# Optimization experiments

Measured on AMD Instinct MI355X. Metric: run time of the kernel, lower is better.

## Reference

```python
import jax, jax.numpy as jnp
import numpy as np

B, D, H, W = 2, 256, 64, 64
NH = 4
EPS = 1e-5


def _ln(x, g, b):
    # LayerNorm over channel dim of NCHW tensor (matches permute->LN(C)->permute)
    mu = jnp.mean(x, axis=1, keepdims=True)
    var = jnp.mean((x - mu) ** 2, axis=1, keepdims=True)
    xn = (x - mu) * jax.lax.rsqrt(var + EPS)
    return xn * g[None, :, None, None] + b[None, :, None, None]


def _conv1x1(x, w, b):
    # w: (out_c, in_c)
    return jnp.einsum('bchw,oc->bohw', x, w) + b[None, :, None, None]


def _dwconv3x3(x, w, b):
    # depthwise 3x3, w: (C, 1, 3, 3)
    y = jax.lax.conv_general_dilated(
        x, w, window_strides=(1, 1), padding='SAME',
        dimension_numbers=('NCHW', 'OIHW', 'NCHW'), feature_group_count=D)
    return y + b[None, :, None, None]


def setup_inputs() -> dict:
    key = jax.random.key(0)
    ks = jax.random.split(key, 12)
    sc = 0.02

    def n(k, shape):
        return jax.random.normal(k, shape, dtype=jnp.float32) * sc

    return {
        'image_embedding': jax.random.normal(ks[0], (B, D, H, W), dtype=jnp.float32),
        'guide': jax.random.normal(ks[1], (B, D, H, W), dtype=jnp.float32),
        'ln1_g': jnp.ones((D,), jnp.float32), 'ln1_b': jnp.zeros((D,), jnp.float32),
        'ln2_g': jnp.ones((D,), jnp.float32), 'ln2_b': jnp.zeros((D,), jnp.float32),
        'qw1': n(ks[2], (D, D)), 'qb1': jnp.zeros((D,), jnp.float32),
        'qw2': n(ks[3], (D, 1, 3, 3)), 'qb2': jnp.zeros((D,), jnp.float32),
        'kw1': n(ks[4], (D, D)), 'kb1': jnp.zeros((D,), jnp.float32),
        'kw2': n(ks[5], (D, 1, 3, 3)), 'kb2': jnp.zeros((D,), jnp.float32),
        'vw1': n(ks[6], (D, D)), 'vb1': jnp.zeros((D,), jnp.float32),
        'vw2': n(ks[7], (D, 1, 3, 3)), 'vb2': jnp.zeros((D,), jnp.float32),
        'ow': n(ks[8], (D, D)), 'ob': jnp.zeros((D,), jnp.float32),
    }


def reference(image_embedding, guide, ln1_g, ln1_b, ln2_g, ln2_b,
              qw1, qb1, qw2, qb2, kw1, kb1, kw2, kb2,
              vw1, vb1, vw2, vb2, ow, ob):
    residual = image_embedding
    x = _ln(image_embedding, ln1_g, ln1_b)
    g = _ln(guide, ln2_g, ln2_b)

    q = _dwconv3x3(_conv1x1(x, qw1, qb1), qw2, qb2)
    k = _dwconv3x3(_conv1x1(g, kw1, kb1), kw2, kb2)
    v = _dwconv3x3(_conv1x1(g, vw1, vb1), vw2, vb2)

    hd = D // NH
    scale = hd ** -0.5

    def to_heads(t):  # (B,C,H,W) -> (B, NH, HW, hd)
        return t.reshape(B, NH, hd, H * W).transpose(0, 1, 3, 2)

    q = to_heads(q) * scale
    k = to_heads(k)
    v = to_heads(v)

    attn = jax.nn.softmax(jnp.einsum('bhnd,bhmd->bhnm', q, k), axis=-1)
    out = jnp.einsum('bhnm,bhmd->bhnd', attn, v)
    out = out.transpose(0, 1, 3, 2).reshape(B, D, H, W)
    out = _conv1x1(out, ow, ob)
    return residual + out
```

## Files before the change

### kernel.cpp

```cpp
#include <hip/hip_runtime.h>
#include <cstdint>
#include <cstddef>

typedef unsigned short u16;
typedef unsigned int u32;
typedef __attribute__((ext_vector_type(8))) short short8;
typedef __attribute__((ext_vector_type(4))) float f32x4;
typedef __attribute__((ext_vector_type(16))) float f32x16;
typedef __attribute__((ext_vector_type(2))) unsigned int u32x2;

#define CD 256
#define HWD 4096
#define NHD 4
#define HDD 64
#define NSPLIT 4

static __device__ __forceinline__ u16 f2b(float f) {
    u32 u = __builtin_bit_cast(u32, f);
    return (u16)((u + 0x7fffu + ((u >> 16) & 1u)) >> 16);
}
static __device__ __forceinline__ float b2f(u16 h) {
    return __builtin_bit_cast(float, (u32)h << 16);
}
static __device__ __forceinline__ u32 pk2(float a, float b) {
    return (u32)f2b(a) | ((u32)f2b(b) << 16);
}
static __device__ __forceinline__ float fexp2(float x) {
#if __has_builtin(__builtin_amdgcn_exp2f)
    return __builtin_amdgcn_exp2f(x);
#else
    return __expf(x * 0.69314718056f);
#endif
}
static __device__ __forceinline__ u32 cvtpk(float lo, float hi) {
    u32 r;
    asm("v_cvt_pk_bf16_f32 %0, %1, %2" : "=v"(r) : "v"(lo), "v"(hi));
    return r;
}
static __device__ __forceinline__ u32x2 plswap(u32 a, u32 b) {
    return __builtin_amdgcn_permlane32_swap(a, b, false, false);
}
static __device__ __forceinline__ void async16(const void* g, void* l) {
    __builtin_amdgcn_global_load_lds(
        (const __attribute__((address_space(1))) unsigned int*)g,
        (__attribute__((address_space(3))) unsigned int*)l,
        16, 0, 0);
}

__global__ __launch_bounds__(256) void ln_transpose(
    const float* __restrict__ x0, const float* __restrict__ x1,
    const float* __restrict__ g0, const float* __restrict__ b0,
    const float* __restrict__ g1, const float* __restrict__ b1,
    const float* __restrict__ qw1, const float* __restrict__ kw1,
    const float* __restrict__ vw1, const float* __restrict__ ow,
    u16* __restrict__ out0, u16* __restrict__ out1, u16* __restrict__ wbf)
{
    int bid = blockIdx.x;
    int tid = threadIdx.x;

    if (bid >= 512) {
        int base = (bid - 512) * 8192 + tid * 32;
        int which = base >> 16;
        int off = base & 65535;
        const float* s = (which == 0) ? qw1 : (which == 1) ? kw1
                       : (which == 2) ? vw1 : ow;
        s += off;
        u16* d = wbf + (size_t)which * 65536 + off;
        #pragma unroll
        for (int j = 0; j < 4; ++j) {
            float4 a = ((const float4*)s)[2 * j];
            float4 b = ((const float4*)s)[2 * j + 1];
            uint4 o;
            o.x = pk2(a.x, a.y); o.y = pk2(a.z, a.w);
            o.z = pk2(b.x, b.y); o.w = pk2(b.z, b.w);
            ((uint4*)d)[j] = o;
        }
        return;
    }

    int t = bid >> 8, b = (bid >> 7) & 1, p0 = (bid & 127) << 5;
    const float* x = t ? x1 : x0;
    const float* g = t ? g1 : g0;
    const float* bb = t ? b1 : b0;
    u16* out = t ? out1 : out0;

    int tx = tid & 31, ty = tid >> 5;
    const float* xb = x + (size_t)b * CD * HWD + p0 + tx;

    __shared__ float red[2][8][32];
    __shared__ u16 T[256][33];

    float xv[32];
    float s = 0.f, sq = 0.f;
    #pragma unroll
    for (int i = 0; i < 32; ++i) {
        float v = xb[(size_t)(ty * 32 + i) * HWD];
        xv[i] = v;
        s += v; sq += v * v;
    }
    red[0][ty][tx] = s; red[1][ty][tx] = sq;
    __syncthreads();
    float st = 0.f, sqt = 0.f;
    #pragma unroll
    for (int j = 0; j < 8; ++j) { st += red[0][j][tx]; sqt += red[1][j][tx]; }
    float mean = st * (1.f / 256.f);
    float var = sqt * (1.f / 256.f) - mean * mean;
    float rstd = rsqrtf(var + 1e-5f);

    #pragma unroll
    for (int i = 0; i < 32; ++i) {
        int c = ty * 32 + i;
        float v = (xv[i] - mean) * rstd * g[c] + bb[c];
        T[c][tx] = f2b(v);
    }
    __syncthreads();

    #pragma unroll
    for (int pass = 0; pass < 4; ++pass) {
        int idx = pass * 256 + tid;
        int p = idx >> 5, cs = (idx & 31) * 8;
        u16 tmp[8];
        #pragma unroll
        for (int j = 0; j < 8; ++j) tmp[j] = T[cs + j][p];
        *(uint4*)&out[((size_t)b * HWD + p0 + p) * CD + cs] = *(const uint4*)tmp;
    }
}

__global__ __launch_bounds__(256) void qkv_gemm(
    const u16* __restrict__ xT, const u16* __restrict__ gT,
    const u16* __restrict__ Wbf,
    const float* __restrict__ qb1, const float* __restrict__ kb1,
    const float* __restrict__ vb1,
    u16* __restrict__ q1, u16* __restrict__ k1, u16* __restrict__ v1)
{
    int z = blockIdx.z;
    int mm = z >> 1, b = z & 1;
    const u16* X    = (mm == 0) ? xT : gT;
    const u16* W    = Wbf + (size_t)mm * 65536;
    const float* Bi = (mm == 0) ? qb1 : (mm == 1) ? kb1 : vb1;
    u16* Y          = (mm == 0) ? q1 : (mm == 1) ? k1 : v1;

    int n0 = blockIdx.x * 128;
    int p0 = blockIdx.y * 32;

    __shared__ u16 As[32][72];
    __shared__ u16 Bs[128][72];

    int tid = threadIdx.x;
    int lane = tid & 63, w = tid >> 6;
    int l15 = lane & 15, quad = lane >> 4;

    f32x4 acc[2][2];
    #pragma unroll
    for (int mi = 0; mi < 2; ++mi)
        #pragma unroll
        for (int nj = 0; nj < 2; ++nj)
            acc[mi][nj] = (f32x4){0.f, 0.f, 0.f, 0.f};

    const u16* Xb = X + (size_t)b * HWD * CD;

    int arow = tid >> 3, aseg = (tid & 7) * 8;
    const u16* agp = Xb + (size_t)(p0 + arow) * CD + aseg;
    int brow = tid >> 1, bkh = (tid & 1) * 32;
    const u16* wgp = W + (size_t)(n0 + brow) * CD + bkh;

    uint4 ra0 = ((const uint4*)agp)[0];
    uint4 rb0 = ((const uint4*)wgp)[0], rb1 = ((const uint4*)wgp)[1];
    uint4 rb2 = ((const uint4*)wgp)[2], rb3 = ((const uint4*)wgp)[3];

    for (int kt = 0; kt < 4; ++kt) {
        __syncthreads();
        *(uint4*)&As[arow][aseg] = ra0;
        *(uint4*)&Bs[brow][bkh] = rb0;
        *(uint4*)&Bs[brow][bkh + 8] = rb1;
        *(uint4*)&Bs[brow][bkh + 16] = rb2;
        *(uint4*)&Bs[brow][bkh + 24] = rb3;
        if (kt < 3) {
            ra0 = *(const uint4*)(agp + (kt + 1) * 64);
            const u16* wg2 = wgp + (kt + 1) * 64;
            rb0 = ((const uint4*)wg2)[0]; rb1 = ((const uint4*)wg2)[1];
            rb2 = ((const uint4*)wg2)[2]; rb3 = ((const uint4*)wg2)[3];
        }
        __syncthreads();

        #pragma unroll
        for (int kk = 0; kk < 2; ++kk) {
            short8 af[2], bf[2];
            #pragma unroll
            for (int mi = 0; mi < 2; ++mi)
                af[mi] = *(const short8*)&As[mi * 16 + l15][kk * 32 + quad * 8];
            #pragma unroll
            for (int nj = 0; nj < 2; ++nj)
                bf[nj] = *(const short8*)&Bs[w * 32 + nj * 16 + l15][kk * 32 + quad * 8];
            #pragma unroll
            for (int mi = 0; mi < 2; ++mi)
                #pragma unroll
                for (int nj = 0; nj < 2; ++nj)
                    acc[mi][nj] = __builtin_amdgcn_mfma_f32_16x16x32_bf16(
                        af[mi], bf[nj], acc[mi][nj], 0, 0, 0);
        }
    }

    u16* Yb = Y + (size_t)b * HWD * CD;
    float bias[2];
    #pragma unroll
    for (int nj = 0; nj < 2; ++nj)
        bias[nj] = Bi[n0 + w * 32 + nj * 16 + l15];
    #pragma unroll
    for (int mi = 0; mi < 2; ++mi) {
        #pragma unroll
        for (int r = 0; r < 4; ++r) {
            int p = p0 + mi * 16 + quad * 4 + r;
            #pragma unroll
            for (int nj = 0; nj < 2; ++nj) {
                int ch = n0 + w * 32 + nj * 16 + l15;
                Yb[(size_t)p * CD + ch] = f2b(acc[mi][nj][r] + bias[nj]);
            }
        }
    }
}

#define LOADROW(r, hh)                                                      \
    if ((hh) < 0 || (hh) >= 64) {                                           \
        _Pragma("unroll") for (int j = 0; j < 18; ++j) r[j] = 0.f;          \
    } else {                                                                \
        const u16* rp = inb + (size_t)((hh) * 64) * CD;                     \
        r[0] = (w0 > 0) ? b2f(rp[(size_t)(w0 - 1) * CD]) : 0.f;             \
        _Pragma("unroll") for (int j = 1; j <= 16; ++j)                     \
            r[j] = b2f(rp[(size_t)(w0 - 1 + j) * CD]);                      \
        r[17] = (w0 < 48) ? b2f(rp[(size_t)(w0 + 16) * CD]) : 0.f;          \
    }

#define CONVROW(hh, ra, rb, rc)                                             \
    {                                                                       \
        float accv[16];                                                     \
        _Pragma("unroll") for (int pi = 0; pi < 16; ++pi)                   \
            accv[pi] = bias                                                 \
              + w9[0] * ra[pi] + w9[1] * ra[pi + 1] + w9[2] * ra[pi + 2]    \
              + w9[3] * rb[pi] + w9[4] * rb[pi + 1] + w9[5] * rb[pi + 2]    \
              + w9[6] * rc[pi] + w9[7] * rc[pi + 1] + w9[8] * rc[pi + 2];   \
        int p0 = (hh) * 64 + w0;                                            \
        if (which == 2) {                                                   \
            u32 w8[8];                                                      \
            _Pragma("unroll") for (int j = 0; j < 8; ++j)                   \
                w8[j] = pk2(accv[2 * j], accv[2 * j + 1]);                  \
            uint4* dst = (uint4*)(Vt + ((size_t)(b * CD + c)) * HWD + p0);  \
            dst[0] = make_uint4(w8[0], w8[1], w8[2], w8[3]);                \
            dst[1] = make_uint4(w8[4], w8[5], w8[6], w8[7]);                \
        } else {                                                            \
            u16* outp = ((which == 0) ? Q : K) + (size_t)b * HWD * CD;      \
            _Pragma("unroll") for (int pi = 0; pi < 16; ++pi)               \
                outp[(size_t)(p0 + pi) * CD + c] = f2b(accv[pi] * oscale);  \
        }                                                                   \
    }

__global__ __launch_bounds__(256) void dwconv_nc(
    const u16* __restrict__ q1, const u16* __restrict__ k1, const u16* __restrict__ v1,
    const float* __restrict__ qw2, const float* __restrict__ qb2,
    const float* __restrict__ kw2, const float* __restrict__ kb2,
    const float* __restrict__ vw2, const float* __restrict__ vb2,
    u16* __restrict__ Q, u16* __restrict__ K, u16* __restrict__ Vt)
{
    int bid = blockIdx.x;
    int which = bid >> 8;
    int rem = bid & 255;
    int b = rem >> 7;
    int hp = (rem >> 2) & 31;
    int ws = rem & 3;
    int h0 = hp * 2, w0 = ws * 16;

    const u16* in = ((which == 0) ? q1 : (which == 1) ? k1 : v1) + (size_t)b * HWD * CD;
    const float* wsrc = (which == 0) ? qw2 : (which == 1) ? kw2 : vw2;
    const float* bsrc = (which == 0) ? qb2 : (which == 1) ? kb2 : vb2;
    float oscale = (which == 0) ? 0.18033688011112042f : 1.0f;

    int c = threadIdx.x;
    float w9[9];
    #pragma unroll
    for (int j = 0; j < 9; ++j) w9[j] = wsrc[c * 9 + j];
    float bias = bsrc[c];

    const u16* inb = in + c;

    float r0[18], r1[18], r2[18];
    LOADROW(r0, h0 - 1)
    LOADROW(r1, h0)
    LOADROW(r2, h0 + 1)
    CONVROW(h0, r0, r1, r2)
    LOADROW(r0, h0 + 2)
    CONVROW(h0 + 1, r1, r2, r0)
}

__global__ __launch_bounds__(256, 2) void attn_kernel(
    const u16* __restrict__ Q, const u16* __restrict__ K,
    const u16* __restrict__ Vt, u16* __restrict__ Opart,
    float* __restrict__ Psum)
{
    int qt = blockIdx.x;
    int bh = blockIdx.y;
    int ks = blockIdx.z;
    int b = bh >> 2, nh = bh & 3;

    __shared__ u16 Ks_[2][64 * 64];
    __shared__ u16 Vs_[2][64 * 64];

    int tid = threadIdx.x;
    int lane = tid & 63, w = tid >> 6;
    int l31 = lane & 31, h = lane >> 5;
    int sw = l31 & 7;

    const u16* Qb = Q + ((size_t)b * HWD) * CD + nh * 64;
    const u16* Kb = K + ((size_t)b * HWD) * CD + nh * 64;
    const u16* Vb = Vt + ((size_t)bh * HDD) * HWD;

    int q0 = qt * 256 + w * 64;

    short8 qf[2][4];
    #pragma unroll
    for (int qi = 0; qi < 2; ++qi)
        #pragma unroll
        for (int si = 0; si < 4; ++si)
            qf[qi][si] = *(const short8*)(Qb +
                (size_t)(q0 + qi * 32 + l31) * CD + si * 16 + h * 8);

    int rr = lane >> 3;
    int gseg = (lane & 7) ^ rr;
    const u16* kgb = Kb + (size_t)(ks * 1024 + w * 16 + rr) * CD + gseg * 8;
    const u16* vgb = Vb + (size_t)(w * 16 + rr) * HWD + ks * 1024 + gseg * 8;

    f32x16 acc[2][2];
    #pragma unroll
    for (int qi = 0; qi < 2; ++qi)
        #pragma unroll
        for (int db = 0; db < 2; ++db)
            #pragma unroll
            for (int r = 0; r < 16; ++r) acc[qi][db][r] = 0.f;
    float psum[2] = {0.f, 0.f};

    #pragma unroll
    for (int j = 0; j < 2; ++j) {
        async16(kgb + (size_t)(j * 8) * CD, &Ks_[0][(w * 16 + j * 8) * 64]);
        async16(vgb + (size_t)(j * 8) * HWD, &Vs_[0][(w * 16 + j * 8) * 64]);
    }

    for (int it = 0; it < 16; ++it) {
        int cur = it & 1;
        __syncthreads();
        if (it + 1 < 16) {
            int nxt = cur ^ 1;
            #pragma unroll
            for (int j = 0; j < 2; ++j) {
                async16(kgb + (size_t)((it + 1) * 64 + j * 8) * CD,
                        &Ks_[nxt][(w * 16 + j * 8) * 64]);
                async16(vgb + (size_t)(j * 8) * HWD + (it + 1) * 64,
                        &Vs_[nxt][(w * 16 + j * 8) * 64]);
            }
        }

        #pragma unroll
        for (int kb = 0; kb < 2; ++kb) {
            short8 kf[4];
            #pragma unroll
            for (int si = 0; si < 4; ++si)
                kf[si] = *(const short8*)&Ks_[cur][(kb * 32 + l31) * 64 +
                                                   (((si * 2 + h) ^ sw) << 3)];
            short8 vf[4];
            #pragma unroll
            for (int dz = 0; dz < 4; ++dz)
                vf[dz] = *(const short8*)&Vs_[cur][((dz >> 1) * 32 + l31) * 64 +
                             ((((kb * 2 + (dz & 1)) * 2 + h) ^ sw) << 3)];

            #pragma unroll
            for (int qi = 0; qi < 2; ++qi) {
                f32x16 st;
                #pragma unroll
                for (int r = 0; r < 16; ++r) st[r] = 0.f;
                __builtin_amdgcn_s_setprio(1);
                #pragma unroll
                for (int si = 0; si < 4; ++si)
                    st = __builtin_amdgcn_mfma_f32_32x32x16_bf16(
                        kf[si], qf[qi][si], st, 0, 0, 0);
                __builtin_amdgcn_s_setprio(0);

                float e[16];
                #pragma unroll
                for (int r = 0; r < 16; ++r) e[r] = fexp2(st[r]);
                #pragma unroll
                for (int r = 0; r < 16; r += 4)
                    psum[qi] += (e[r] + e[r + 1]) + (e[r + 2] + e[r + 3]);

                u32 wv[8];
                #pragma unroll
                for (int m = 0; m < 8; ++m) wv[m] = cvtpk(e[2 * m], e[2 * m + 1]);
                u32x2 s02 = plswap(wv[0], wv[2]);
                u32x2 s13 = plswap(wv[1], wv[3]);
                u32x2 s46 = plswap(wv[4], wv[6]);
                u32x2 s57 = plswap(wv[5], wv[7]);
                union { u32 u[4]; short8 s8; } p0_, p1_;
                p0_.u[0] = s02.x; p0_.u[1] = s13.x; p0_.u[2] = s02.y; p0_.u[3] = s13.y;
                p1_.u[0] = s46.x; p1_.u[1] = s57.x; p1_.u[2] = s46.y; p1_.u[3] = s57.y;

                __builtin_amdgcn_s_setprio(1);
                acc[qi][0] = __builtin_amdgcn_mfma_f32_32x32x16_bf16(
                    p0_.s8, vf[0], acc[qi][0], 0, 0, 0);
                acc[qi][0] = __builtin_amdgcn_mfma_f32_32x32x16_bf16(
                    p1_.s8, vf[1], acc[qi][0], 0, 0, 0);
                acc[qi][1] = __builtin_amdgcn_mfma_f32_32x32x16_bf16(
                    p0_.s8, vf[2], acc[qi][1], 0, 0, 0);
                acc[qi][1] = __builtin_amdgcn_mfma_f32_32x32x16_bf16(
                    p1_.s8, vf[3], acc[qi][1], 0, 0, 0);
                __builtin_amdgcn_s_setprio(0);
            }
        }
    }

    u16* Ob = Opart + (((size_t)ks * 8 + bh) * HWD) * HDD;
    #pragma unroll
    for (int qi = 0; qi < 2; ++qi)
        #pragma unroll
        for (int db = 0; db < 2; ++db)
            #pragma unroll
            for (int r = 0; r < 16; ++r) {
                int n = q0 + qi * 32 + (r & 3) + 8 * (r >> 2) + 4 * h;
                Ob[(size_t)n * HDD + db * 32 + l31] = f2b(acc[qi][db][r]);
            }

    float* Pb = Psum + ((size_t)ks * 8 + bh) * HWD + q0;
    #pragma unroll
    for (int qi = 0; qi < 2; ++qi) {
        float s = psum[qi] + __shfl_xor(psum[qi], 32);
        if (lane < 32) Pb[qi * 32 + lane] = s;
    }
}

__global__ __launch_bounds__(256) void out_gemm(
    const u16* __restrict__ Wo, const float* __restrict__ Bi,
    const u16* __restrict__ Opart, const float* __restrict__ Psum,
    const float* __restrict__ residual, float* __restrict__ out)
{
    int b = blockIdx.z;
    int m0 = blockIdx.y * 64;
    int n0 = blockIdx.x * 32;

    __shared__ u16 As[64][40];
    __shared__ u16 Bs[32][40];

    int tid = threadIdx.x;
    int lane = tid & 63, w = tid >> 6;
    int wm = w >> 1, wn = w & 1;
    int l15 = lane & 15, quad = lane >> 4;

    f32x4 acc[2];
    #pragma unroll
    for (int mi = 0; mi < 2; ++mi)
        acc[mi] = (f32x4){0.f, 0.f, 0.f, 0.f};

    int arow = tid >> 2, aseg = (tid & 3) * 8;
    const u16* wgp = Wo + (size_t)(m0 + arow) * CD + aseg;
    int brow = tid >> 3, bseg = (tid & 7) * 4;
    int pn = n0 + brow;

    uint4 ra = *(const uint4*)wgp;

    uint2 ro[NSPLIT]; float rinv;
    {
        int c = bseg;
        int bh = b * 4 + (c >> 6), d0 = c & 63;
        float p = 0.f;
        #pragma unroll
        for (int s = 0; s < NSPLIT; ++s) {
            ro[s] = *(const uint2*)&Opart[(((size_t)s * 8 + bh) * HWD + pn) * HDD + d0];
            p += Psum[((size_t)s * 8 + bh) * HWD + pn];
        }
        rinv = 1.f / p;
    }

    for (int kt = 0; kt < 8; ++kt) {
        __syncthreads();
        *(uint4*)&As[arow][aseg] = ra;
        {
            float v[4];
            #pragma unroll
            for (int j = 0; j < 4; ++j) v[j] = 0.f;
            #pragma unroll
            for (int s = 0; s < NSPLIT; ++s) {
                u16 t[4];
                *(uint2*)t = ro[s];
                #pragma unroll
                for (int j = 0; j < 4; ++j) v[j] += b2f(t[j]);
            }
            uint2 bb;
            bb.x = pk2(v[0] * rinv, v[1] * rinv);
            bb.y = pk2(v[2] * rinv, v[3] * rinv);
            *(uint2*)&Bs[brow][bseg] = bb;
        }
        if (kt < 7) {
            ra = *(const uint4*)(wgp + (kt + 1) * 32);
            int c = (kt + 1) * 32 + bseg;
            int bh = b * 4 + (c >> 6), d0 = c & 63;
            float p = 0.f;
            #pragma unroll
            for (int s = 0; s < NSPLIT; ++s) {
                ro[s] = *(const uint2*)&Opart[(((size_t)s * 8 + bh) * HWD + pn) * HDD + d0];
                p += Psum[((size_t)s * 8 + bh) * HWD + pn];
            }
            rinv = 1.f / p;
        }
        __syncthreads();

        short8 af[2], bf;
        #pragma unroll
        for (int mi = 0; mi < 2; ++mi)
            af[mi] = *(const short8*)&As[wm * 32 + mi * 16 + l15][quad * 8];
        bf = *(const short8*)&Bs[wn * 16 + l15][quad * 8];
        #pragma unroll
        for (int mi = 0; mi < 2; ++mi)
            acc[mi] = __builtin_amdgcn_mfma_f32_16x16x32_bf16(
                af[mi], bf, acc[mi], 0, 0, 0);
    }

    #pragma unroll
    for (int mi = 0; mi < 2; ++mi) {
        int mb = m0 + wm * 32 + mi * 16 + quad * 4;
        #pragma unroll
        for (int r = 0; r < 4; ++r) {
            float bias = Bi[mb + r];
            const float* res = residual + (size_t)(b * CD + mb + r) * HWD;
            float* o = out + (size_t)(b * CD + mb + r) * HWD;
            int n = n0 + wn * 16 + l15;
            o[n] = acc[mi][r] + bias + res[n];
        }
    }
}

extern "C" void kernel_launch(void* const* d_in, const int* in_sizes, int n_in,
                              void* d_out, int out_size, void* d_ws, size_t ws_size,
                              hipStream_t stream) {
    (void)in_sizes; (void)n_in; (void)out_size; (void)ws_size;

    const float* image = (const float*)d_in[0];
    const float* guide = (const float*)d_in[1];
    const float* ln1_g = (const float*)d_in[2];
    const float* ln1_b = (const float*)d_in[3];
    const float* ln2_g = (const float*)d_in[4];
    const float* ln2_b = (const float*)d_in[5];
    const float* qw1 = (const float*)d_in[6];
    const float* qb1 = (const float*)d_in[7];
    const float* qw2 = (const float*)d_in[8];
    const float* qb2 = (const float*)d_in[9];
    const float* kw1 = (const float*)d_in[10];
    const float* kb1 = (const float*)d_in[11];
    const float* kw2 = (const float*)d_in[12];
    const float* kb2 = (const float*)d_in[13];
    const float* vw1 = (const float*)d_in[14];
    const float* vb1 = (const float*)d_in[15];
    const float* vw2 = (const float*)d_in[16];
    const float* vb2 = (const float*)d_in[17];
    const float* ow  = (const float*)d_in[18];
    const float* ob  = (const float*)d_in[19];
    float* out = (float*)d_out;

    char* ws = (char*)d_ws;
    u16* xT    = (u16*)(ws + (size_t)0  * (1 << 20));
    u16* gT    = (u16*)(ws + (size_t)4  * (1 << 20));
    u16* q1    = (u16*)(ws + (size_t)8  * (1 << 20));
    u16* k1    = (u16*)(ws + (size_t)12 * (1 << 20));
    u16* v1    = (u16*)(ws + (size_t)16 * (1 << 20));
    u16* Qh    = (u16*)(ws + (size_t)20 * (1 << 20));
    u16* Kh    = (u16*)(ws + (size_t)24 * (1 << 20));
    u16* Vt    = (u16*)(ws + (size_t)28 * (1 << 20));
    u16*   Opart = (u16*)(ws + (size_t)0  * (1 << 20));
    float* Psum  = (float*)(ws + (size_t)18 * (1 << 20));
    u16*   Wbf   = (u16*)(ws + (size_t)33 * (1 << 20));

    ln_transpose<<<dim3(544), dim3(256), 0, stream>>>(
        image, guide, ln1_g, ln1_b, ln2_g, ln2_b,
        qw1, kw1, vw1, ow, xT, gT, Wbf);

    qkv_gemm<<<dim3(2, 128, 6), dim3(256), 0, stream>>>(
        xT, gT, Wbf, qb1, kb1, vb1, q1, k1, v1);

    dwconv_nc<<<dim3(768), dim3(256), 0, stream>>>(
        q1, k1, v1, qw2, qb2, kw2, kb2, vw2, vb2, Qh, Kh, Vt);

    attn_kernel<<<dim3(16, 8, NSPLIT), dim3(256), 0, stream>>>(Qh, Kh, Vt, Opart, Psum);

    out_gemm<<<dim3(128, 4, 2), dim3(256), 0, stream>>>(
        Wbf + (size_t)3 * 65536, ob, Opart, Psum, image, out);
}
```

Baseline: 174.6 us.

## Double-buffer QKV GEMM tiles with async global-to-LDS loads and XOR swizzle

The QKV projection GEMM now copies its A and B tiles straight from global memory into LDS with async 16-byte loads into two ping-pong buffers. This removes the register staging step and one barrier per k-step, so the next tile's loads overlap with the MFMA work on the current one. The padded LDS rows are replaced by an XOR-swizzled unpadded layout to avoid bank conflicts on the fragment reads. The swizzle is applied on the global-address side, and correctness depends on the barrier also waiting for the async loads to finish.

```diff
diff --git a/kernel.cpp b/kernel.cpp
--- a/kernel.cpp
+++ b/kernel.cpp
@@ -143,12 +143,22 @@
     int n0 = blockIdx.x * 128;
     int p0 = blockIdx.y * 32;
 
-    __shared__ u16 As[32][72];
-    __shared__ u16 Bs[128][72];
+    __shared__ u16 As[2][32 * 64];
+    __shared__ u16 Bs[2][128 * 64];
 
     int tid = threadIdx.x;
     int lane = tid & 63, w = tid >> 6;
     int l15 = lane & 15, quad = lane >> 4;
+    int sw = l15 & 7;
+
+    int srow = tid >> 3;
+    int sseg = tid & 7;
+    const u16* Xb = X + (size_t)b * HWD * CD;
+    const u16* agp = Xb + (size_t)(p0 + srow) * CD + (sseg ^ (srow & 7)) * 8;
+    const u16* wgp0 = W + (size_t)(n0 +  0 + srow) * CD + (sseg ^ (srow & 7)) * 8;
+    const u16* wgp1 = W + (size_t)(n0 + 32 + srow) * CD + (sseg ^ (srow & 7)) * 8;
+    const u16* wgp2 = W + (size_t)(n0 + 64 + srow) * CD + (sseg ^ (srow & 7)) * 8;
+    const u16* wgp3 = W + (size_t)(n0 + 96 + srow) * CD + (sseg ^ (srow & 7)) * 8;
 
     f32x4 acc[2][2];
     #pragma unroll
@@ -157,41 +167,39 @@
         for (int nj = 0; nj < 2; ++nj)
             acc[mi][nj] = (f32x4){0.f, 0.f, 0.f, 0.f};
 
-    const u16* Xb = X + (size_t)b * HWD * CD;
-
-    int arow = tid >> 3, aseg = (tid & 7) * 8;
-    const u16* agp = Xb + (size_t)(p0 + arow) * CD + aseg;
-    int brow = tid >> 1, bkh = (tid & 1) * 32;
-    const u16* wgp = W + (size_t)(n0 + brow) * CD + bkh;
-
-    uint4 ra0 = ((const uint4*)agp)[0];
-    uint4 rb0 = ((const uint4*)wgp)[0], rb1 = ((const uint4*)wgp)[1];
-    uint4 rb2 = ((const uint4*)wgp)[2], rb3 = ((const uint4*)wgp)[3];
+    async16(agp, &As[0][w * 512]);
+    async16(wgp0, &Bs[0][0 * 2048 + w * 512]);
+    async16(wgp1, &Bs[0][1 * 2048 + w * 512]);
+    async16(wgp2, &Bs[0][2 * 2048 + w * 512]);
+    async16(wgp3, &Bs[0][3 * 2048 + w * 512]);
 
     for (int kt = 0; kt < 4; ++kt) {
+        int cur = kt & 1;
         __syncthreads();
-        *(uint4*)&As[arow][aseg] = ra0;
-        *(uint4*)&Bs[brow][bkh] = rb0;
-        *(uint4*)&Bs[brow][bkh + 8] = rb1;
-        *(uint4*)&Bs[brow][bkh + 16] = rb2;
-        *(uint4*)&Bs[brow][bkh + 24] = rb3;
         if (kt < 3) {
-            ra0 = *(const uint4*)(agp + (kt + 1) * 64);
-            const u16* wg2 = wgp + (kt + 1) * 64;
-            rb0 = ((const uint4*)wg2)[0]; rb1 = ((const uint4*)wg2)[1];
-            rb2 = ((const uint4*)wg2)[2]; rb3 = ((const uint4*)wg2)[3];
-        }
-        __syncthreads();
+            int nxt = cur ^ 1;
+            async16(agp + (kt + 1) * 64, &As[nxt][w * 512]);
+            async16(wgp0 + (kt + 1) * 64, &Bs[nxt][0 * 2048 + w * 512]);
+            async16(wgp1 + (kt + 1) * 64, &Bs[nxt][1 * 2048 + w * 512]);
+            async16(wgp2 + (kt + 1) * 64, &Bs[nxt][2 * 2048 + w * 512]);
+            async16(wgp3 + (kt + 1) * 64, &Bs[nxt][3 * 2048 + w * 512]);
+        }
 
         #pragma unroll
         for (int kk = 0; kk < 2; ++kk) {
             short8 af[2], bf[2];
             #pragma unroll
-            for (int mi = 0; mi < 2; ++mi)
-                af[mi] = *(const short8*)&As[mi * 16 + l15][kk * 32 + quad * 8];
-            #pragma unroll
-            for (int nj = 0; nj < 2; ++nj)
-                bf[nj] = *(const short8*)&Bs[w * 32 + nj * 16 + l15][kk * 32 + quad * 8];
+            for (int mi = 0; mi < 2; ++mi) {
+                int row = mi * 16 + l15;
+                af[mi] = *(const short8*)&As[cur][row * 64 +
+                                                  (((kk * 4 + quad) ^ sw) << 3)];
+            }
+            #pragma unroll
+            for (int nj = 0; nj < 2; ++nj) {
+                int row = w * 32 + nj * 16 + l15;
+                bf[nj] = *(const short8*)&Bs[cur][row * 64 +
+                                                  (((kk * 4 + quad) ^ sw) << 3)];
+            }
             #pragma unroll
             for (int mi = 0; mi < 2; ++mi)
                 #pragma unroll
```

New measurement: 173.6 us, median of 2. About the same (-0.6%).

## Fuse LayerNorm into QKV GEMM and move output weight conversion to dwconv

Applied to the files above, without the earlier changes.

LayerNorm is now computed inside the QKV GEMM. Each block normalizes its 32-pixel tile over all 256 channels into a swizzled LDS buffer, and fp32 weights are converted to bf16 on the fly, so the separate transpose kernel and its xT/gT round trip go away. Conversion of the output-projection weight moves to extra blocks in the dwconv launch. This saves one kernel launch and the intermediate global traffic. In exchange, the LN is recomputed redundantly across the two n-blocks, across the k and v GEMMs, and across batches per z, and weight conversion is repeated per block.

```diff
diff --git a/kernel.cpp b/kernel.cpp
--- a/kernel.cpp
+++ b/kernel.cpp
@@ -47,108 +47,75 @@
         16, 0, 0);
 }
 
-__global__ __launch_bounds__(256) void ln_transpose(
+__global__ __launch_bounds__(256) void ln_qkv_gemm(
     const float* __restrict__ x0, const float* __restrict__ x1,
     const float* __restrict__ g0, const float* __restrict__ b0,
     const float* __restrict__ g1, const float* __restrict__ b1,
     const float* __restrict__ qw1, const float* __restrict__ kw1,
-    const float* __restrict__ vw1, const float* __restrict__ ow,
-    u16* __restrict__ out0, u16* __restrict__ out1, u16* __restrict__ wbf)
-{
-    int bid = blockIdx.x;
-    int tid = threadIdx.x;
-
-    if (bid >= 512) {
-        int base = (bid - 512) * 8192 + tid * 32;
-        int which = base >> 16;
-        int off = base & 65535;
-        const float* s = (which == 0) ? qw1 : (which == 1) ? kw1
-                       : (which == 2) ? vw1 : ow;
-        s += off;
-        u16* d = wbf + (size_t)which * 65536 + off;
-        #pragma unroll
-        for (int j = 0; j < 4; ++j) {
-            float4 a = ((const float4*)s)[2 * j];
-            float4 b = ((const float4*)s)[2 * j + 1];
-            uint4 o;
-            o.x = pk2(a.x, a.y); o.y = pk2(a.z, a.w);
-            o.z = pk2(b.x, b.y); o.w = pk2(b.z, b.w);
-            ((uint4*)d)[j] = o;
-        }
-        return;
-    }
-
-    int t = bid >> 8, b = (bid >> 7) & 1, p0 = (bid & 127) << 5;
-    const float* x = t ? x1 : x0;
-    const float* g = t ? g1 : g0;
-    const float* bb = t ? b1 : b0;
-    u16* out = t ? out1 : out0;
-
-    int tx = tid & 31, ty = tid >> 5;
-    const float* xb = x + (size_t)b * CD * HWD + p0 + tx;
-
-    __shared__ float red[2][8][32];
-    __shared__ u16 T[256][33];
-
-    float xv[32];
-    float s = 0.f, sq = 0.f;
-    #pragma unroll
-    for (int i = 0; i < 32; ++i) {
-        float v = xb[(size_t)(ty * 32 + i) * HWD];
-        xv[i] = v;
-        s += v; sq += v * v;
-    }
-    red[0][ty][tx] = s; red[1][ty][tx] = sq;
-    __syncthreads();
-    float st = 0.f, sqt = 0.f;
-    #pragma unroll
-    for (int j = 0; j < 8; ++j) { st += red[0][j][tx]; sqt += red[1][j][tx]; }
-    float mean = st * (1.f / 256.f);
-    float var = sqt * (1.f / 256.f) - mean * mean;
-    float rstd = rsqrtf(var + 1e-5f);
-
-    #pragma unroll
-    for (int i = 0; i < 32; ++i) {
-        int c = ty * 32 + i;
-        float v = (xv[i] - mean) * rstd * g[c] + bb[c];
-        T[c][tx] = f2b(v);
-    }
-    __syncthreads();
-
-    #pragma unroll
-    for (int pass = 0; pass < 4; ++pass) {
-        int idx = pass * 256 + tid;
-        int p = idx >> 5, cs = (idx & 31) * 8;
-        u16 tmp[8];
-        #pragma unroll
-        for (int j = 0; j < 8; ++j) tmp[j] = T[cs + j][p];
-        *(uint4*)&out[((size_t)b * HWD + p0 + p) * CD + cs] = *(const uint4*)tmp;
-    }
-}
-
-__global__ __launch_bounds__(256) void qkv_gemm(
-    const u16* __restrict__ xT, const u16* __restrict__ gT,
-    const u16* __restrict__ Wbf,
+    const float* __restrict__ vw1,
     const float* __restrict__ qb1, const float* __restrict__ kb1,
     const float* __restrict__ vb1,
     u16* __restrict__ q1, u16* __restrict__ k1, u16* __restrict__ v1)
 {
     int z = blockIdx.z;
     int mm = z >> 1, b = z & 1;
-    const u16* X    = (mm == 0) ? xT : gT;
-    const u16* W    = Wbf + (size_t)mm * 65536;
+    const float* x  = (mm == 0) ? x0 : x1;
+    const float* g  = (mm == 0) ? g0 : g1;
+    const float* bb = (mm == 0) ? b0 : b1;
+    const float* W  = (mm == 0) ? qw1 : (mm == 1) ? kw1 : vw1;
     const float* Bi = (mm == 0) ? qb1 : (mm == 1) ? kb1 : vb1;
     u16* Y          = (mm == 0) ? q1 : (mm == 1) ? k1 : v1;
 
     int n0 = blockIdx.x * 128;
     int p0 = blockIdx.y * 32;
 
-    __shared__ u16 As[32][72];
+    __shared__ u16 As[32 * 256];
     __shared__ u16 Bs[128][72];
+    __shared__ float red[2][8][32];
 
     int tid = threadIdx.x;
     int lane = tid & 63, w = tid >> 6;
     int l15 = lane & 15, quad = lane >> 4;
+    int sw = l15 & 7;
+
+    int tx = tid & 31, ty = tid >> 5;
+    const float* xb = x + (size_t)b * CD * HWD + p0 + tx;
+    float xv[32];
+    float s = 0.f, sq = 0.f;
+    #pragma unroll
+    for (int i = 0; i < 32; ++i) {
+        float v = xb[(size_t)(ty * 32 + i) * HWD];
+        xv[i] = v; s += v; sq += v * v;
+    }
+    red[0][ty][tx] = s; red[1][ty][tx] = sq;
+    __syncthreads();
+    float st = 0.f, sqt = 0.f;
+    #pragma unroll
+    for (int j = 0; j < 8; ++j) { st += red[0][j][tx]; sqt += red[1][j][tx]; }
+    float mean = st * (1.f / 256.f);
+    float var = sqt * (1.f / 256.f) - mean * mean;
+    float rstd = rsqrtf(var + 1e-5f);
+
+    #pragma unroll
+    for (int j = 0; j < 4; ++j) {
+        float v[8];
+        #pragma unroll
+        for (int e = 0; e < 8; ++e) {
+            int c = ty * 32 + j * 8 + e;
+            v[e] = (xv[j * 8 + e] - mean) * rstd * g[c] + bb[c];
+        }
+        uint4 o;
+        o.x = pk2(v[0], v[1]); o.y = pk2(v[2], v[3]);
+        o.z = pk2(v[4], v[5]); o.w = pk2(v[6], v[7]);
+        int chunk = (ty * 4 + j) ^ (tx & 7);
+        *(uint4*)&As[tx * 256 + chunk * 8] = o;
+    }
+
+    int brow = tid >> 1, bkh = (tid & 1) * 32;
+    const float* wgp = W + (size_t)(n0 + brow) * CD + bkh;
+    float4 rw[8];
+    #pragma unroll
+    for (int j = 0; j < 8; ++j) rw[j] = ((const float4*)wgp)[j];
 
     f32x4 acc[2][2];
     #pragma unroll
@@ -157,29 +124,27 @@
         for (int nj = 0; nj < 2; ++nj)
             acc[mi][nj] = (f32x4){0.f, 0.f, 0.f, 0.f};
 
-    const u16* Xb = X + (size_t)b * HWD * CD;
-
-    int arow = tid >> 3, aseg = (tid & 7) * 8;
-    const u16* agp = Xb + (size_t)(p0 + arow) * CD + aseg;
-    int brow = tid >> 1, bkh = (tid & 1) * 32;
-    const u16* wgp = W + (size_t)(n0 + brow) * CD + bkh;
-
-    uint4 ra0 = ((const uint4*)agp)[0];
-    uint4 rb0 = ((const uint4*)wgp)[0], rb1 = ((const uint4*)wgp)[1];
-    uint4 rb2 = ((const uint4*)wgp)[2], rb3 = ((const uint4*)wgp)[3];
-
     for (int kt = 0; kt < 4; ++kt) {
         __syncthreads();
-        *(uint4*)&As[arow][aseg] = ra0;
-        *(uint4*)&Bs[brow][bkh] = rb0;
-        *(uint4*)&Bs[brow][bkh + 8] = rb1;
-        *(uint4*)&Bs[brow][bkh + 16] = rb2;
-        *(uint4*)&Bs[brow][bkh + 24] = rb3;
+        {
+            uint4 qa, qb;
+            qa.x = pk2(rw[0].x, rw[0].y); qa.y = pk2(rw[0].z, rw[0].w);
+            qa.z = pk2(rw[1].x, rw[1].y); qa.w = pk2(rw[1].z, rw[1].w);
+            qb.x = pk2(rw[2].x, rw[2].y); qb.y = pk2(rw[2].z, rw[2].w);
+            qb.z = pk2(rw[3].x, rw[3].y); qb.w = pk2(rw[3].z, rw[3].w);
+            *(uint4*)&Bs[brow][bkh] = qa;
+            *(uint4*)&Bs[brow][bkh + 8] = qb;
+            qa.x = pk2(rw[4].x, rw[4].y); qa.y = pk2(rw[4].z, rw[4].w);
+            qa.z = pk2(rw[5].x, rw[5].y); qa.w = pk2(rw[5].z, rw[5].w);
+            qb.x = pk2(rw[6].x, rw[6].y); qb.y = pk2(rw[6].z, rw[6].w);
+            qb.z = pk2(rw[7].x, rw[7].y); qb.w = pk2(rw[7].z, rw[7].w);
+            *(uint4*)&Bs[brow][bkh + 16] = qa;
+            *(uint4*)&Bs[brow][bkh + 24] = qb;
+        }
         if (kt < 3) {
-            ra0 = *(const uint4*)(agp + (kt + 1) * 64);
-            const u16* wg2 = wgp + (kt + 1) * 64;
-            rb0 = ((const uint4*)wg2)[0]; rb1 = ((const uint4*)wg2)[1];
-            rb2 = ((const uint4*)wg2)[2]; rb3 = ((const uint4*)wg2)[3];
+            const float* wg2 = wgp + (kt + 1) * 64;
+            #pragma unroll
+            for (int j = 0; j < 8; ++j) rw[j] = ((const float4*)wg2)[j];
         }
         __syncthreads();
 
@@ -187,8 +152,11 @@
         for (int kk = 0; kk < 2; ++kk) {
             short8 af[2], bf[2];
             #pragma unroll
-            for (int mi = 0; mi < 2; ++mi)
-                af[mi] = *(const short8*)&As[mi * 16 + l15][kk * 32 + quad * 8];
+            for (int mi = 0; mi < 2; ++mi) {
+                int row = mi * 16 + l15;
+                int c = kt * 8 + kk * 4 + quad;
+                af[mi] = *(const short8*)&As[row * 256 + ((c ^ sw) << 3)];
+            }
             #pragma unroll
             for (int nj = 0; nj < 2; ++nj)
                 bf[nj] = *(const short8*)&Bs[w * 32 + nj * 16 + l15][kk * 32 + quad * 8];
@@ -259,9 +227,28 @@
     const float* __restrict__ qw2, const float* __restrict__ qb2,
     const float* __restrict__ kw2, const float* __restrict__ kb2,
     const float* __restrict__ vw2, const float* __restrict__ vb2,
+    const float* __restrict__ ow, u16* __restrict__ wbf,
     u16* __restrict__ Q, u16* __restrict__ K, u16* __restrict__ Vt)
 {
     int bid = blockIdx.x;
+    int tid = threadIdx.x;
+
+    if (bid >= 768) {
+        int base = (bid - 768) * 8192 + tid * 32;
+        const float* s = ow + base;
+        u16* d = wbf + base;
+        #pragma unroll
+        for (int j = 0; j < 4; ++j) {
+            float4 a = ((const float4*)s)[2 * j];
+            float4 b = ((const float4*)s)[2 * j + 1];
+            uint4 o;
+            o.x = pk2(a.x, a.y); o.y = pk2(a.z, a.w);
+            o.z = pk2(b.x, b.y); o.w = pk2(b.z, b.w);
+            ((uint4*)d)[j] = o;
+        }
+        return;
+    }
+
     int which = bid >> 8;
     int rem = bid & 255;
     int b = rem >> 7;
@@ -274,7 +261,7 @@
     const float* bsrc = (which == 0) ? qb2 : (which == 1) ? kb2 : vb2;
     float oscale = (which == 0) ? 0.18033688011112042f : 1.0f;
 
-    int c = threadIdx.x;
+    int c = tid;
     float w9[9];
     #pragma unroll
     for (int j = 0; j < 9; ++j) w9[j] = wsrc[c * 9 + j];
@@ -561,8 +548,6 @@
     float* out = (float*)d_out;
 
     char* ws = (char*)d_ws;
-    u16* xT    = (u16*)(ws + (size_t)0  * (1 << 20));
-    u16* gT    = (u16*)(ws + (size_t)4  * (1 << 20));
     u16* q1    = (u16*)(ws + (size_t)8  * (1 << 20));
     u16* k1    = (u16*)(ws + (size_t)12 * (1 << 20));
     u16* v1    = (u16*)(ws + (size_t)16 * (1 << 20));
@@ -573,18 +558,15 @@
     float* Psum  = (float*)(ws + (size_t)18 * (1 << 20));
     u16*   Wbf   = (u16*)(ws + (size_t)33 * (1 << 20));
 
-    ln_transpose<<<dim3(544), dim3(256), 0, stream>>>(
+    ln_qkv_gemm<<<dim3(2, 128, 6), dim3(256), 0, stream>>>(
         image, guide, ln1_g, ln1_b, ln2_g, ln2_b,
-        qw1, kw1, vw1, ow, xT, gT, Wbf);
-
-    qkv_gemm<<<dim3(2, 128, 6), dim3(256), 0, stream>>>(
-        xT, gT, Wbf, qb1, kb1, vb1, q1, k1, v1);
-
-    dwconv_nc<<<dim3(768), dim3(256), 0, stream>>>(
-        q1, k1, v1, qw2, qb2, kw2, kb2, vw2, vb2, Qh, Kh, Vt);
+        qw1, kw1, vw1, qb1, kb1, vb1, q1, k1, v1);
+
+    dwconv_nc<<<dim3(776), dim3(256), 0, stream>>>(
+        q1, k1, v1, qw2, qb2, kw2, kb2, vw2, vb2, ow, Wbf, Qh, Kh, Vt);
 
     attn_kernel<<<dim3(16, 8, NSPLIT), dim3(256), 0, stream>>>(Qh, Kh, Vt, Opart, Psum);
 
     out_gemm<<<dim3(128, 4, 2), dim3(256), 0, stream>>>(
-        Wbf + (size_t)3 * 65536, ob, Opart, Psum, image, out);
-}
+        Wbf, ob, Opart, Psum, image, out);
+}
```

New measurement: 188.4 us. 7.9% more time.
